# Kernel tuning notes

Hardware: AMD Instinct MI355X
Metric: run time of the kernel (lower is better)

The kernel has to match this reference:

```python
import jax, jax.numpy as jnp
import numpy as np

B, C, D, H, W = 2, 128, 16, 96, 96


def setup_inputs() -> dict:
    key = jax.random.key(0)
    k1, k2 = jax.random.split(key)
    x = jax.random.normal(k1, (B, C, D, H, W), dtype=jnp.float32)
    gamma = jax.random.uniform(k2, (1,), dtype=jnp.float32)
    return {"x": x, "gamma": gamma}


def reference(x, gamma):
    b, c, d, h, w = x.shape
    n = d * h * w
    q = x.reshape(b, c, n)                      # [B,C,N] query==key==value
    # energy: [B,C,C] = q @ q^T
    energy = jnp.einsum('bcn,bdn->bcd', q, q)
    # EnergyMaxNorm: rowwise max (AdaptiveMaxPool1d(1) over last dim) minus energy
    e_max = jnp.max(energy, axis=-1, keepdims=True)
    energy = e_max - energy
    attn = jax.nn.softmax(energy, axis=-1)      # [B,C,C]
    out = jnp.einsum('bcd,bdn->bcn', attn, q)   # [B,C,N]
    out = out.reshape(b, c, d, h, w)
    # gamma-scaled residual fusion (modulation_type 'addition')
    return x + gamma[0] * out
```

## Files before the change

kernel.cpp:

```cpp
#include <hip/hip_runtime.h>

typedef unsigned short u16;
typedef unsigned int u32;
typedef __attribute__((ext_vector_type(8))) short short8;
typedef __attribute__((ext_vector_type(4))) float f32x4;
typedef __attribute__((ext_vector_type(4))) u16 u16x4;

#define NBATCH 2
#define NC 128
#define NN 147456
#define CH 64
#define NCH (NN / CH)
#define G1_PARTS 256
#define N3_PER_B 1152

__device__ __forceinline__ u16 bf16rne(float f) {
  u32 u = __builtin_bit_cast(u32, f);
  return (u16)((u + 0x7FFFu + ((u >> 16) & 1u)) >> 16);
}
__device__ __forceinline__ float bf2f(u16 h) {
  u32 u = ((u32)h) << 16;
  return __builtin_bit_cast(float, u);
}
__device__ __forceinline__ void split2(float f, u16& h, u16& g) {
  u32 u = __builtin_bit_cast(u32, f);
  h = (u16)(u >> 16);
  float hf = __builtin_bit_cast(float, u & 0xFFFF0000u);
  g = bf16rne(f - hf);
}

__global__ __launch_bounds__(256, 2)
void gram_k(const float* __restrict__ x, float* __restrict__ part) {
  __shared__ u16 hi[2][128 * CH];
  __shared__ u16 lo[2][128 * CH];
  const int tid = threadIdx.x;
  const int bid = blockIdx.x;
  const int b   = bid >> 8;
  const int pi  = bid & 255;
  const int w   = tid >> 6;
  const int l   = tid & 63;
  const int grp = l >> 4;
  const int lr  = l & 15;
  const int swz = (lr & 7) << 3;
  const float* xb = x + (size_t)b * NC * NN;

  const int col4 = tid & 15;
  const int r0   = tid >> 4;

  f32x4 acc[2][8];
#pragma unroll
  for (int i = 0; i < 2; ++i)
#pragma unroll
    for (int j = 0; j < 8; ++j) acc[i][j] = (f32x4){0.f, 0.f, 0.f, 0.f};

  float4 v[8];

  auto issue = [&](int ch) {
    const int k0 = ch * CH + (col4 << 2);
#pragma unroll
    for (int j = 0; j < 8; ++j)
      v[j] = *(const float4*)(xb + (size_t)(r0 + (j << 4)) * NN + k0);
  };
  auto stage = [&](int bb) {
    u16* H = &hi[bb][0];
    u16* L = &lo[bb][0];
#pragma unroll
    for (int j = 0; j < 8; ++j) {
      const int row = r0 + (j << 4);
      const int idx = (row << 6) + ((col4 << 2) ^ ((row & 7) << 3));
      u16 h0, h1, h2, h3, g0, g1, g2, g3;
      split2(v[j].x, h0, g0); split2(v[j].y, h1, g1);
      split2(v[j].z, h2, g2); split2(v[j].w, h3, g3);
      *(u16x4*)(H + idx) = (u16x4){h0, h1, h2, h3};
      *(u16x4*)(L + idx) = (u16x4){g0, g1, g2, g3};
    }
  };
  const int m0 = (w << 5) + lr;
  const int m1 = m0 + 16;
  auto mma = [&](int bb) {
    const u16* H = &hi[bb][0];
    const u16* L = &lo[bb][0];
#pragma unroll
    for (int kk = 0; kk < CH; kk += 32) {
      const int kv = (kk + (grp << 3)) ^ swz;
      const short8 Ah0 = *(const short8*)(H + (m0 << 6) + kv);
      const short8 Al0 = *(const short8*)(L + (m0 << 6) + kv);
      const short8 Ah1 = *(const short8*)(H + (m1 << 6) + kv);
      const short8 Al1 = *(const short8*)(L + (m1 << 6) + kv);
#pragma unroll
      for (int nt = 0; nt < 8; ++nt) {
        const int nr  = (nt << 4) + lr;
        const int bix = (nr << 6) + kv;
        const short8 Bh = *(const short8*)(H + bix);
        const short8 Bl = *(const short8*)(L + bix);
        acc[0][nt] = __builtin_amdgcn_mfma_f32_16x16x32_bf16(Ah0, Bh, acc[0][nt], 0, 0, 0);
        acc[0][nt] = __builtin_amdgcn_mfma_f32_16x16x32_bf16(Ah0, Bl, acc[0][nt], 0, 0, 0);
        acc[0][nt] = __builtin_amdgcn_mfma_f32_16x16x32_bf16(Al0, Bh, acc[0][nt], 0, 0, 0);
        acc[1][nt] = __builtin_amdgcn_mfma_f32_16x16x32_bf16(Ah1, Bh, acc[1][nt], 0, 0, 0);
        acc[1][nt] = __builtin_amdgcn_mfma_f32_16x16x32_bf16(Ah1, Bl, acc[1][nt], 0, 0, 0);
        acc[1][nt] = __builtin_amdgcn_mfma_f32_16x16x32_bf16(Al1, Bh, acc[1][nt], 0, 0, 0);
      }
    }
  };

  issue(pi);
  stage(0);
  __syncthreads();

  const int NITER = NCH / G1_PARTS;
  for (int i = 0; i < NITER; ++i) {
    if (i + 1 < NITER) issue(pi + (i + 1) * G1_PARTS);
    mma(i & 1);
    if (i + 1 < NITER) stage((i + 1) & 1);
    __syncthreads();
  }

  float* pb = part + (size_t)bid * 16384;
#pragma unroll
  for (int mt = 0; mt < 2; ++mt)
#pragma unroll
    for (int nt = 0; nt < 8; ++nt)
#pragma unroll
      for (int r = 0; r < 4; ++r) {
        const int row = (w << 5) + (mt << 4) + (grp << 2) + r;
        const int col = (nt << 4) + lr;
        pb[(row << 7) + col] = acc[mt][nt][r];
      }
}

__global__ __launch_bounds__(128)
void soft_k(const float* __restrict__ part, u16* __restrict__ attn) {
  const int b = blockIdx.x >> 7;
  const int c = blockIdx.x & 127;
  const int d = threadIdx.x;
  __shared__ float red[128];
  float e = 0.f;
  const float* p0 = part + ((size_t)(b * G1_PARTS) << 14) + (c << 7) + d;
  for (int p = 0; p < G1_PARTS; ++p) e += p0[(size_t)p << 14];
  red[d] = e;
  __syncthreads();
#pragma unroll
  for (int s = 64; s > 0; s >>= 1) {
    if (d < s) red[d] = fminf(red[d], red[d + s]);
    __syncthreads();
  }
  const float emin = red[0];
  __syncthreads();
  const float pr = __expf(emin - e);
  red[d] = pr;
  __syncthreads();
#pragma unroll
  for (int s = 64; s > 0; s >>= 1) {
    if (d < s) red[d] += red[d + s];
    __syncthreads();
  }
  const float inv = 1.f / red[0];
  attn[(((size_t)b) << 14) + (c << 7) + d] = bf16rne(pr * inv);
}

__global__ __launch_bounds__(256, 2)
void pv_k(const float* __restrict__ x, const u16* __restrict__ attn,
          const float* __restrict__ gamma, float* __restrict__ out) {
  __shared__ float xt[128 * 128];
  const int tid = threadIdx.x;
  const int bid = blockIdx.x;
  const int b   = bid / N3_PER_B;
  const int nb  = (bid % N3_PER_B) << 7;
  const int w = tid >> 6, l = tid & 63, grp = l >> 4, lr = l & 15;
  const size_t bbase = (size_t)b * NC * NN;
  const float* xb = x + bbase;
  const u16* ab = attn + ((size_t)b << 14);

  float4 sv[16];
#pragma unroll
  for (int j = 0; j < 16; ++j) {
    const int f4  = tid + (j << 8);
    const int row = f4 >> 5, fc = f4 & 31;
    sv[j] = *(const float4*)(xb + (size_t)row * NN + nb + (fc << 2));
  }
#pragma unroll
  for (int j = 0; j < 16; ++j) {
    const int f4  = tid + (j << 8);
    const int row = f4 >> 5, fc = f4 & 31;
    const int fsw = fc ^ (((row >> 3) & 1) << 2);
    *(float4*)(xt + (row << 7) + (fsw << 2)) = sv[j];
  }
  __syncthreads();

  f32x4 acc[8][2];
#pragma unroll
  for (int i = 0; i < 8; ++i) {
    acc[i][0] = (f32x4){0.f, 0.f, 0.f, 0.f};
    acc[i][1] = (f32x4){0.f, 0.f, 0.f, 0.f};
  }

  const int nwt = (w << 5) + lr;

#pragma unroll
  for (int kk = 0; kk < 4; ++kk) {
    const int KK = kk << 5;
    short8 A[8];
#pragma unroll
    for (int mt = 0; mt < 8; ++mt)
      A[mt] = *(const short8*)(ab + (((mt << 4) + lr) << 7) + KK + (grp << 3));

    const int dbase = KK + (grp << 3);
#pragma unroll
    for (int t = 0; t < 2; ++t) {
      const int nx = (nwt + (t << 4)) ^ ((grp & 1) << 4);
      const float* bp = xt + (dbase << 7) + nx;
      float f[8];
#pragma unroll
      for (int i = 0; i < 8; ++i) f[i] = bp[i << 7];
      u16 h[8], g[8];
#pragma unroll
      for (int i = 0; i < 8; ++i) split2(f[i], h[i], g[i]);
      const short8 Bh = (short8){(short)h[0], (short)h[1], (short)h[2], (short)h[3],
                                 (short)h[4], (short)h[5], (short)h[6], (short)h[7]};
      const short8 Bl = (short8){(short)g[0], (short)g[1], (short)g[2], (short)g[3],
                                 (short)g[4], (short)g[5], (short)g[6], (short)g[7]};
#pragma unroll
      for (int mt = 0; mt < 8; ++mt) {
        acc[mt][t] = __builtin_amdgcn_mfma_f32_16x16x32_bf16(A[mt], Bh, acc[mt][t], 0, 0, 0);
        acc[mt][t] = __builtin_amdgcn_mfma_f32_16x16x32_bf16(A[mt], Bl, acc[mt][t], 0, 0, 0);
      }
    }
  }

  const float gm = gamma[0];
#pragma unroll
  for (int mt = 0; mt < 8; ++mt)
#pragma unroll
    for (int t = 0; t < 2; ++t)
#pragma unroll
      for (int r = 0; r < 4; ++r) {
        const int c = (mt << 4) + (grp << 2) + r;
        const int n = nwt + (t << 4);
        const float rd = xt[(c << 7) + (n ^ ((grp >> 1) << 4))];
        out[bbase + (size_t)c * NN + nb + n] = rd + gm * acc[mt][t][r];
      }
}

extern "C" void kernel_launch(void* const* d_in, const int* in_sizes, int n_in,
                              void* d_out, int out_size, void* d_ws, size_t ws_size,
                              hipStream_t stream) {
  (void)in_sizes; (void)n_in; (void)out_size; (void)ws_size;
  const float* x     = (const float*)d_in[0];
  const float* gamma = (const float*)d_in[1];
  float* out  = (float*)d_out;
  u16*   attn = (u16*)d_ws;
  float* part = out;

  gram_k<<<dim3(2 * G1_PARTS), dim3(256), 0, stream>>>(x, part);
  soft_k<<<dim3(2 * 128),      dim3(128), 0, stream>>>(part, attn);
  pv_k  <<<dim3(2 * N3_PER_B), dim3(256), 0, stream>>>(x, attn, gamma, out);
}
```

Baseline: 121.3 us.

## Make PV kernel persistent with double-buffered 64-column tiles

The PV kernel now launches 512 persistent blocks. Each block loops over 9 tiles of 64 columns, with the LDS tile double-buffered so the next tile's global loads overlap the current tile's MFMA work and residual store. This replaces the previous one-shot grid of 2304 blocks, each loading a 128-column tile before computing. It removes the exposed load latency of the non-pipelined design, at the cost of fewer blocks for latency hiding and a smaller per-tile MFMA reuse.

After: 171.6 us. 41.5% more time.

```diff
diff --git a/kernel.cpp b/kernel.cpp
--- a/kernel.cpp
+++ b/kernel.cpp
@@ -12,7 +12,10 @@
 #define CH 64
 #define NCH (NN / CH)
 #define G1_PARTS 256
-#define N3_PER_B 1152
+#define T3N 64
+#define T3_PER_B (NN / T3N)
+#define T3_BLOCKS 512
+#define T3_ITERS 9
 
 __device__ __forceinline__ u16 bf16rne(float f) {
   u32 u = __builtin_bit_cast(u32, f);
@@ -161,57 +164,56 @@
 __global__ __launch_bounds__(256, 2)
 void pv_k(const float* __restrict__ x, const u16* __restrict__ attn,
           const float* __restrict__ gamma, float* __restrict__ out) {
-  __shared__ float xt[128 * 128];
+  __shared__ float xt[2][128 * T3N];
   const int tid = threadIdx.x;
   const int bid = blockIdx.x;
-  const int b   = bid / N3_PER_B;
-  const int nb  = (bid % N3_PER_B) << 7;
   const int w = tid >> 6, l = tid & 63, grp = l >> 4, lr = l & 15;
-  const size_t bbase = (size_t)b * NC * NN;
-  const float* xb = x + bbase;
-  const u16* ab = attn + ((size_t)b << 14);
-
-  float4 sv[16];
-#pragma unroll
-  for (int j = 0; j < 16; ++j) {
-    const int f4  = tid + (j << 8);
-    const int row = f4 >> 5, fc = f4 & 31;
-    sv[j] = *(const float4*)(xb + (size_t)row * NN + nb + (fc << 2));
-  }
-#pragma unroll
-  for (int j = 0; j < 16; ++j) {
-    const int f4  = tid + (j << 8);
-    const int row = f4 >> 5, fc = f4 & 31;
-    const int fsw = fc ^ (((row >> 3) & 1) << 2);
-    *(float4*)(xt + (row << 7) + (fsw << 2)) = sv[j];
-  }
-  __syncthreads();
-
-  f32x4 acc[8][2];
-#pragma unroll
-  for (int i = 0; i < 8; ++i) {
-    acc[i][0] = (f32x4){0.f, 0.f, 0.f, 0.f};
-    acc[i][1] = (f32x4){0.f, 0.f, 0.f, 0.f};
-  }
-
-  const int nwt = (w << 5) + lr;
-
-#pragma unroll
-  for (int kk = 0; kk < 4; ++kk) {
-    const int KK = kk << 5;
-    short8 A[8];
-#pragma unroll
-    for (int mt = 0; mt < 8; ++mt)
-      A[mt] = *(const short8*)(ab + (((mt << 4) + lr) << 7) + KK + (grp << 3));
-
-    const int dbase = KK + (grp << 3);
-#pragma unroll
-    for (int t = 0; t < 2; ++t) {
-      const int nx = (nwt + (t << 4)) ^ ((grp & 1) << 4);
-      const float* bp = xt + (dbase << 7) + nx;
+  const int nw = (w << 4) + lr;
+  const float gm = gamma[0];
+
+  const int r0 = tid >> 4;
+  const int fc = tid & 15;
+
+  float4 sv[8];
+
+  auto issue = [&](int tau) {
+    const int b = tau / T3_PER_B;
+    const size_t base = (size_t)b * NC * NN + (size_t)(tau - b * T3_PER_B) * T3N;
+#pragma unroll
+    for (int j = 0; j < 8; ++j)
+      sv[j] = *(const float4*)(x + base + (size_t)(r0 + (j << 4)) * NN + (fc << 2));
+  };
+  auto stage = [&](int bb) {
+    float* X = &xt[bb][0];
+#pragma unroll
+    for (int j = 0; j < 8; ++j) {
+      const int row = r0 + (j << 4);
+      const int c4  = fc ^ (((row >> 3) & 1) << 2);
+      *(float4*)(X + (row << 6) + (c4 << 2)) = sv[j];
+    }
+  };
+  auto work = [&](int tau, int bb) {
+    const int b = tau / T3_PER_B;
+    const size_t obase = (size_t)b * NC * NN + (size_t)(tau - b * T3_PER_B) * T3N;
+    const u16* ab = attn + ((size_t)b << 14);
+    const float* X = &xt[bb][0];
+
+    f32x4 acc[8];
+#pragma unroll
+    for (int i = 0; i < 8; ++i) acc[i] = (f32x4){0.f, 0.f, 0.f, 0.f};
+
+#pragma unroll
+    for (int kk = 0; kk < 4; ++kk) {
+      const int KK = kk << 5;
+      const int dbase = KK + (grp << 3);
+      short8 A[8];
+#pragma unroll
+      for (int mt = 0; mt < 8; ++mt)
+        A[mt] = *(const short8*)(ab + (((mt << 4) + lr) << 7) + KK + (grp << 3));
+      const int nsw = nw ^ ((grp & 1) << 4);
       float f[8];
 #pragma unroll
-      for (int i = 0; i < 8; ++i) f[i] = bp[i << 7];
+      for (int i = 0; i < 8; ++i) f[i] = X[((dbase + i) << 6) + nsw];
       u16 h[8], g[8];
 #pragma unroll
       for (int i = 0; i < 8; ++i) split2(f[i], h[i], g[i]);
@@ -221,24 +223,31 @@
                                  (short)g[4], (short)g[5], (short)g[6], (short)g[7]};
 #pragma unroll
       for (int mt = 0; mt < 8; ++mt) {
-        acc[mt][t] = __builtin_amdgcn_mfma_f32_16x16x32_bf16(A[mt], Bh, acc[mt][t], 0, 0, 0);
-        acc[mt][t] = __builtin_amdgcn_mfma_f32_16x16x32_bf16(A[mt], Bl, acc[mt][t], 0, 0, 0);
-      }
-    }
-  }
-
-  const float gm = gamma[0];
-#pragma unroll
-  for (int mt = 0; mt < 8; ++mt)
-#pragma unroll
-    for (int t = 0; t < 2; ++t)
+        acc[mt] = __builtin_amdgcn_mfma_f32_16x16x32_bf16(A[mt], Bh, acc[mt], 0, 0, 0);
+        acc[mt] = __builtin_amdgcn_mfma_f32_16x16x32_bf16(A[mt], Bl, acc[mt], 0, 0, 0);
+      }
+    }
+
+#pragma unroll
+    for (int mt = 0; mt < 8; ++mt)
 #pragma unroll
       for (int r = 0; r < 4; ++r) {
         const int c = (mt << 4) + (grp << 2) + r;
-        const int n = nwt + (t << 4);
-        const float rd = xt[(c << 7) + (n ^ ((grp >> 1) << 4))];
-        out[bbase + (size_t)c * NN + nb + n] = rd + gm * acc[mt][t][r];
-      }
+        const float rd = X[(c << 6) + (nw ^ (((c >> 3) & 1) << 4))];
+        out[obase + (size_t)c * NN + nw] = rd + gm * acc[mt][r];
+      }
+  };
+
+  issue(bid);
+  stage(0);
+  __syncthreads();
+
+  for (int i = 0; i < T3_ITERS; ++i) {
+    if (i + 1 < T3_ITERS) issue(bid + (i + 1) * T3_BLOCKS);
+    work(bid + i * T3_BLOCKS, i & 1);
+    if (i + 1 < T3_ITERS) stage((i + 1) & 1);
+    __syncthreads();
+  }
 }
 
 extern "C" void kernel_launch(void* const* d_in, const int* in_sizes, int n_in,
@@ -253,5 +262,5 @@
 
   gram_k<<<dim3(2 * G1_PARTS), dim3(256), 0, stream>>>(x, part);
   soft_k<<<dim3(2 * 128),      dim3(128), 0, stream>>>(part, attn);
-  pv_k  <<<dim3(2 * N3_PER_B), dim3(256), 0, stream>>>(x, attn, gamma, out);
-}
+  pv_k  <<<dim3(T3_BLOCKS),    dim3(256), 0, stream>>>(x, attn, gamma, out);
+}
```
